# Kernel optimization log

Measured on AMD Instinct MI355X. Metric: run time of the kernel, lower is better.

The kernel has to match this reference:

```python
import jax, jax.numpy as jnp
import numpy as np
import math

D_MODEL = 2048
N_HEADS = 16
D_HEAD = D_MODEL // N_HEADS  # 128, also the RoPE dim
ROPE_BASE = 10000.0
B, T = 2, 2048


def _rope_cos_sin(seq_len, dim, dtype):
    inv_freq = 1.0 / (ROPE_BASE ** (jnp.arange(0, dim, 2, dtype=jnp.float32) / dim))
    t = jnp.arange(seq_len, dtype=jnp.float32)
    freqs = jnp.einsum('i,j->ij', t, inv_freq)          # [T, dim/2]
    emb = jnp.concatenate((freqs, freqs), axis=-1)       # [T, dim]  (half-concat layout, as in source)
    cos = jnp.cos(emb)[None, None, :, :].astype(dtype)   # [1,1,T,dim]
    sin = jnp.sin(emb)[None, None, :, :].astype(dtype)
    return cos, sin


def _apply_rot(x, cos, sin, dim):
    # interleaved pair rotation, faithful to the torch code
    x1 = x[..., 0:dim:2]
    x2 = x[..., 1:dim:2]
    x_rot = jnp.stack((-x2, x1), axis=-1).reshape(x.shape[:-1] + (dim,))
    return x[..., :dim] * cos + x_rot * sin


def setup_inputs() -> dict:
    key = jax.random.key(0)
    k1, k2, k3 = jax.random.split(key, 3)
    x = jax.random.normal(k1, (B, T, D_MODEL), dtype=jnp.float32)
    # causal additive mask, broadcastable to [B,H,T,T]
    neg = jnp.finfo(jnp.float32).min / 2
    causal = jnp.triu(jnp.full((T, T), neg, dtype=jnp.float32), k=1)
    mask = causal[None, None, :, :]
    Wqkv = jax.random.normal(k2, (D_MODEL, 3 * D_MODEL), dtype=jnp.float32) * (1.0 / math.sqrt(D_MODEL))
    bqkv = jnp.zeros((3 * D_MODEL,), dtype=jnp.float32)
    Wo = jax.random.normal(k3, (D_MODEL, D_MODEL), dtype=jnp.float32) * (1.0 / math.sqrt(D_MODEL))
    bo = jnp.zeros((D_MODEL,), dtype=jnp.float32)
    return {"x": x, "mask": mask, "Wqkv": Wqkv, "bqkv": bqkv, "Wo": Wo, "bo": bo}


def reference(x, mask, Wqkv, bqkv, Wo, bo):
    Bx, Tx, C = x.shape
    qkv = x @ Wqkv + bqkv                                     # [B,T,3C]
    qkv = qkv.reshape(Bx, Tx, 3, N_HEADS, D_HEAD)
    qkv = jnp.transpose(qkv, (2, 0, 3, 1, 4))                 # [3,B,H,T,dh]
    q, k, v = qkv[0], qkv[1], qkv[2]
    cos, sin = _rope_cos_sin(Tx, D_HEAD, x.dtype)
    q = _apply_rot(q, cos, sin, D_HEAD)
    k = _apply_rot(k, cos, sin, D_HEAD)
    att = jnp.einsum('bhqd,bhkd->bhqk', q, k) / math.sqrt(D_HEAD)
    att = att + mask
    att = jax.nn.softmax(att, axis=-1)
    y = jnp.einsum('bhqk,bhkd->bhqd', att, v)                 # [B,H,T,dh]
    y = jnp.transpose(y, (0, 2, 1, 3)).reshape(Bx, Tx, C)
    return y @ Wo + bo
```

## Files before the change

kernel.cpp:

```cpp
#include <hip/hip_runtime.h>
#include <stdint.h>

#define TDIM 2048
#define DMODEL 2048
#define NHEADS 16
#define DHEAD 128
#define NBATCH 2
#define NTOK (NBATCH * TDIM)
#define NQKV (3 * DMODEL)
#define BHTOT (NBATCH * NHEADS)

typedef unsigned short u16;
typedef __attribute__((ext_vector_type(8))) short bf16x8;
typedef __attribute__((ext_vector_type(4))) float f32x4;
typedef __attribute__((ext_vector_type(4))) int i32x4;

__device__ __forceinline__ u16 f2bf(float f) {
  union { float f; uint32_t u; } v; v.f = f;
  uint32_t u = v.u + 0x7fffu + ((v.u >> 16) & 1u);
  return (u16)(u >> 16);
}
__device__ __forceinline__ float bf2f(u16 h) {
  union { uint32_t u; float f; } v; v.u = ((uint32_t)h) << 16;
  return v.f;
}

#define GLOAD16(g, l)                                                        \
  __builtin_amdgcn_global_load_lds(                                          \
      (const __attribute__((address_space(1))) void*)(g),                    \
      (__attribute__((address_space(3))) void*)(l), 16, 0, 0)

__global__ void rope_table_kernel(float* __restrict__ ct, float* __restrict__ st) {
  int idx = blockIdx.x * 256 + threadIdx.x;
  int t = idx >> 6, m = idx & 63;
  float inv = expf(-(float)m * (9.210340371976184f / 64.0f));
  float ang = (float)t * inv;
  ct[idx] = cosf(ang);
  st[idx] = sinf(ang);
}

__global__ void convert_kernel(const float* __restrict__ in, u16* __restrict__ out) {
  int i = blockIdx.x * 256 + threadIdx.x;
  float4 v = ((const float4*)in)[i];
  ushort4 o;
  o.x = f2bf(v.x); o.y = f2bf(v.y); o.z = f2bf(v.z); o.w = f2bf(v.w);
  ((ushort4*)out)[i] = o;
}

__global__ __launch_bounds__(256) void transpose_convert_kernel(
    const float* __restrict__ in, u16* __restrict__ out, int K, int N) {
  __shared__ u16 tile[32][33];
  int n0 = blockIdx.x * 32, k0 = blockIdx.y * 32;
  int tx = threadIdx.x, ty = threadIdx.y;
  #pragma unroll
  for (int q = 0; q < 4; q++) {
    int k = ty + q * 8;
    tile[k][tx] = f2bf(in[(size_t)(k0 + k) * N + n0 + tx]);
  }
  __syncthreads();
  #pragma unroll
  for (int q = 0; q < 4; q++) {
    int n = ty + q * 8;
    out[(size_t)(n0 + n) * K + k0 + tx] = tile[tx][n];
  }
}

__global__ __launch_bounds__(256) void vtrans_kernel(
    const u16* __restrict__ Vtmp, u16* __restrict__ Vt) {
  __shared__ u16 tile[32][33];
  int bh = blockIdx.z;
  int t0 = blockIdx.x * 32, d0 = blockIdx.y * 32;
  int tx = threadIdx.x, ty = threadIdx.y;
  const u16* src = Vtmp + (size_t)bh * TDIM * DHEAD;
  u16* dst = Vt + (size_t)bh * DHEAD * TDIM;
  #pragma unroll
  for (int q = 0; q < 4; q++) {
    int t = ty + q * 8;
    tile[t][tx] = src[(size_t)(t0 + t) * DHEAD + d0 + tx];
  }
  __syncthreads();
  #pragma unroll
  for (int q = 0; q < 4; q++) {
    int d = ty + q * 8;
    dst[(size_t)(d0 + d) * TDIM + t0 + tx] = tile[tx][d];
  }
}

template <int MODE>
__global__ __launch_bounds__(512, 2) void gemm_bt_kernel(
    const u16* __restrict__ A, const u16* __restrict__ Bt,
    const float* __restrict__ bias,
    u16* __restrict__ q_out, u16* __restrict__ k_out, u16* __restrict__ v_out,
    float* __restrict__ f_out,
    const float* __restrict__ ct, const float* __restrict__ st, int K) {
  __shared__ __attribute__((aligned(128))) char lds[3][49152];
  const int tid = threadIdx.x;
  const int lane = tid & 63, w = tid >> 6;
  const int wr = w >> 2, wc = w & 3;
  const int g = lane >> 4, c = lane & 15;
  const int m0 = blockIdx.x * 128, n0 = blockIdx.y * 256;
  const size_t rowb = (size_t)K * 2;
  const int NKT = K >> 6;

  const char* sSrc[6]; int sDst[6];
  #pragma unroll
  for (int p = 0; p < 2; p++) {
    int o = p * 8192 + tid * 16;
    int row = o >> 7, j = (o >> 4) & 7;
    sSrc[p] = (const char*)A + (size_t)(m0 + row) * rowb + ((j ^ (row & 7)) << 4);
    sDst[p] = o;
  }
  #pragma unroll
  for (int p = 0; p < 4; p++) {
    int o = p * 8192 + tid * 16;
    int row = o >> 7, j = (o >> 4) & 7;
    sSrc[2 + p] = (const char*)Bt + (size_t)(n0 + row) * rowb + ((j ^ (row & 7)) << 4);
    sDst[2 + p] = 16384 + o;
  }

#define STAGE3(bufp, kt, base)                                               \
  {                                                                          \
    const size_t kb_ = (size_t)(kt) * 128;                                   \
    _Pragma("unroll") for (int p_ = 0; p_ < 3; p_++)                         \
        GLOAD16(sSrc[(base) + p_] + kb_, (bufp) + sDst[(base) + p_]);        \
  }

  int aRd[4][2], bRd[4][2];
  #pragma unroll
  for (int m = 0; m < 4; m++) {
    #pragma unroll
    for (int ks = 0; ks < 2; ks++) {
      int arow = wr * 64 + m * 16 + c;
      aRd[m][ks] = arow * 128 + (((ks * 4 + g) ^ (c & 7)) << 4);
      int brow = wc * 64 + m * 16 + c;
      bRd[m][ks] = 16384 + brow * 128 + (((ks * 4 + g) ^ (c & 7)) << 4);
    }
  }

  const f32x4 zero = {0.f, 0.f, 0.f, 0.f};
  f32x4 acc[4][4];
  #pragma unroll
  for (int m = 0; m < 4; m++)
    #pragma unroll
    for (int n = 0; n < 4; n++) acc[m][n] = zero;

  STAGE3(lds[0], 0, 0); STAGE3(lds[0], 0, 3);
  STAGE3(lds[1], 1, 0); STAGE3(lds[1], 1, 3);
  asm volatile("s_waitcnt vmcnt(6)" ::: "memory");
  __builtin_amdgcn_s_barrier();
  __builtin_amdgcn_sched_barrier(0);

  for (int kt = 0; kt < NKT; kt++) {
    char* bp = lds[kt % 3];
    char* sp = lds[(kt + 2) % 3];
    const bool do_stage = (kt + 2 < NKT);

    {
      bf16x8 afr[4], bfr[4];
      #pragma unroll
      for (int n = 0; n < 4; n++) bfr[n] = *(const bf16x8*)(bp + bRd[n][0]);
      #pragma unroll
      for (int m = 0; m < 4; m++) afr[m] = *(const bf16x8*)(bp + aRd[m][0]);
      if (do_stage) STAGE3(sp, kt + 2, 0);
      __builtin_amdgcn_s_barrier();
      asm volatile("s_waitcnt lgkmcnt(0)" ::: "memory");
      __builtin_amdgcn_sched_barrier(0);
      __builtin_amdgcn_s_setprio(1);
      #pragma unroll
      for (int m = 0; m < 4; m++)
        #pragma unroll
        for (int n = 0; n < 4; n++)
          acc[m][n] = __builtin_amdgcn_mfma_f32_16x16x32_bf16(
              afr[m], bfr[n], acc[m][n], 0, 0, 0);
      __builtin_amdgcn_s_setprio(0);
      __builtin_amdgcn_s_barrier();
      __builtin_amdgcn_sched_barrier(0);
    }

    {
      bf16x8 afr[4], bfr[4];
      #pragma unroll
      for (int n = 0; n < 4; n++) bfr[n] = *(const bf16x8*)(bp + bRd[n][1]);
      #pragma unroll
      for (int m = 0; m < 4; m++) afr[m] = *(const bf16x8*)(bp + aRd[m][1]);
      if (do_stage) STAGE3(sp, kt + 2, 3);
      if (do_stage) {
        asm volatile("s_waitcnt vmcnt(6)" ::: "memory");
      } else {
        asm volatile("s_waitcnt vmcnt(0)" ::: "memory");
      }
      __builtin_amdgcn_s_barrier();
      asm volatile("s_waitcnt lgkmcnt(0)" ::: "memory");
      __builtin_amdgcn_sched_barrier(0);
      __builtin_amdgcn_s_setprio(1);
      #pragma unroll
      for (int m = 0; m < 4; m++)
        #pragma unroll
        for (int n = 0; n < 4; n++)
          acc[m][n] = __builtin_amdgcn_mfma_f32_16x16x32_bf16(
              afr[m], bfr[n], acc[m][n], 0, 0, 0);
      __builtin_amdgcn_s_setprio(0);
      __builtin_amdgcn_s_barrier();
      __builtin_amdgcn_sched_barrier(0);
    }
  }
#undef STAGE3

  #pragma unroll
  for (int m = 0; m < 4; m++) {
    #pragma unroll
    for (int n = 0; n < 4; n++) {
      int gcol = n0 + wc * 64 + n * 16 + c;
      float bv = bias[gcol];
      float val[4];
      #pragma unroll
      for (int r = 0; r < 4; r++) val[r] = acc[m][n][r] + bv;
      if (MODE == 0) {
        int s = n0 >> 11;
        int rem = gcol & 2047;
        int h = rem >> 7, d = rem & 127;
        int b0 = (m0 + wr * 64 + m * 16) >> 11;
        size_t hb = (((size_t)(b0 * NHEADS + h)) * TDIM) * DHEAD + d;
        if (s == 2) {
          #pragma unroll
          for (int r = 0; r < 4; r++) {
            int t = (m0 + wr * 64 + m * 16 + g * 4 + r) & (TDIM - 1);
            v_out[hb + (size_t)t * DHEAD] = f2bf(val[r]);
          }
        } else {
          int mf = gcol & 63;
          float sgn = (c & 1) ? 1.0f : -1.0f;
          u16* dst = (s == 0) ? q_out : k_out;
          float qs = (s == 0) ? 0.08838834764831845f : 1.0f;
          #pragma unroll
          for (int r = 0; r < 4; r++) {
            float part = __shfl_xor(val[r], 1, 64);
            int t = (m0 + wr * 64 + m * 16 + g * 4 + r) & (TDIM - 1);
            float cs = ct[t * 64 + mf], sn = st[t * 64 + mf];
            float rot = (val[r] * cs + sgn * part * sn) * qs;
            dst[hb + (size_t)t * DHEAD] = f2bf(rot);
          }
        }
      } else {
        #pragma unroll
        for (int r = 0; r < 4; r++) {
          int grow = m0 + wr * 64 + m * 16 + g * 4 + r;
          f_out[(size_t)grow * DMODEL + gcol] = val[r];
        }
      }
    }
  }
}

__global__ __launch_bounds__(256) void attn_kernel(
    const u16* __restrict__ Q, const u16* __restrict__ K,
    const u16* __restrict__ Vt, u16* __restrict__ Yattn) {
  __shared__ u16 Ks[2][64 * 128];
  __shared__ u16 Vs[2][128 * 64];
  __shared__ u16 Ps[4][16 * 64];
  const int tid = threadIdx.x, lane = tid & 63, w = tid >> 6;
  const int g = lane >> 4, c = lane & 15;
  const int bh = blockIdx.y, b = bh >> 4, h = bh & 15;
  const u16* Qp = Q + (size_t)bh * TDIM * DHEAD;
  const u16* Kp = K + (size_t)bh * TDIM * DHEAD;
  const u16* Vp = Vt + (size_t)bh * DHEAD * TDIM;
  const f32x4 zero = {0.f, 0.f, 0.f, 0.f};

  for (int half = 0; half < 2; half++) {
    const int qt = half ? (31 - (int)blockIdx.x) : (int)blockIdx.x;
    const int qb = qt * 64 + w * 16;

    bf16x8 qf[4];
    #pragma unroll
    for (int kc = 0; kc < 4; kc++)
      qf[kc] = *(const bf16x8*)(Qp + (size_t)(qb + c) * DHEAD + kc * 32 + g * 8);

    f32x4 po[8];
    #pragma unroll
    for (int df = 0; df < 8; df++) po[df] = zero;
    float mrun[4], lrun[4];
    #pragma unroll
    for (int r = 0; r < 4; r++) { mrun[r] = -1e30f; lrun[r] = 0.f; }

    const int nt = qt + 1;

    {
      #pragma unroll
      for (int p = 0; p < 4; p++) {
        int off = p * 4096 + tid * 16;
        int kr = off >> 8, kc4 = (off & 255) >> 4;
        GLOAD16((const char*)Kp + (size_t)kr * 256 + ((kc4 ^ (kr & 7)) << 4),
                (char*)Ks[0] + off);
        int vr = off >> 7, vc4 = (off & 127) >> 4;
        GLOAD16((const char*)Vp + (size_t)vr * (TDIM * 2) + ((vc4 ^ (vr & 7)) << 4),
                (char*)Vs[0] + off);
      }
    }
    __syncthreads();

    int cur = 0;
    for (int t = 0; t < nt; t++) {
      if (t + 1 < nt) {
        int kv0n = (t + 1) * 64;
        char* KsN = (char*)Ks[cur ^ 1];
        char* VsN = (char*)Vs[cur ^ 1];
        #pragma unroll
        for (int p = 0; p < 4; p++) {
          int off = p * 4096 + tid * 16;
          int kr = off >> 8, kc4 = (off & 255) >> 4;
          GLOAD16((const char*)Kp + (size_t)(kv0n + kr) * 256 +
                      ((kc4 ^ (kr & 7)) << 4),
                  KsN + off);
          int vr = off >> 7, vc4 = (off & 127) >> 4;
          GLOAD16((const char*)Vp + (size_t)vr * (TDIM * 2) + (size_t)kv0n * 2 +
                      ((vc4 ^ (vr & 7)) << 4),
                  VsN + off);
        }
      }

      const u16* KsC = Ks[cur];
      const u16* VsC = Vs[cur];
      const int kv0 = t * 64;

      f32x4 sa[4];
      #pragma unroll
      for (int n = 0; n < 4; n++) sa[n] = zero;
      __builtin_amdgcn_s_setprio(1);
      #pragma unroll
      for (int n = 0; n < 4; n++) {
        int krow = n * 16 + c;
        #pragma unroll
        for (int kc = 0; kc < 4; kc++) {
          int kb = (kc * 32 + g * 8) * 2;
          bf16x8 kf = *(const bf16x8*)((const char*)KsC + krow * 256 +
                                       (kb ^ ((krow & 7) << 4)));
          sa[n] = __builtin_amdgcn_mfma_f32_16x16x32_bf16(qf[kc], kf, sa[n], 0, 0, 0);
        }
      }
      __builtin_amdgcn_s_setprio(0);

      if (kv0 + 63 > qb) {
        #pragma unroll
        for (int n = 0; n < 4; n++) {
          int col = kv0 + n * 16 + c;
          #pragma unroll
          for (int r = 0; r < 4; r++) {
            int qrow = qb + g * 4 + r;
            if (col > qrow) sa[n][r] = -1e30f;
          }
        }
      }

      float pvals[4][4];
      #pragma unroll
      for (int r = 0; r < 4; r++) {
        float vmax = fmaxf(fmaxf(sa[0][r], sa[1][r]), fmaxf(sa[2][r], sa[3][r]));
        #pragma unroll
        for (int d = 1; d < 16; d <<= 1) vmax = fmaxf(vmax, __shfl_xor(vmax, d, 64));
        float mnew = fmaxf(mrun[r], vmax);
        float scale = __expf(mrun[r] - mnew);
        float rs = 0.f;
        #pragma unroll
        for (int n = 0; n < 4; n++) {
          float p = __expf(sa[n][r] - mnew);
          pvals[r][n] = p;
          rs += p;
        }
        #pragma unroll
        for (int d = 1; d < 16; d <<= 1) rs += __shfl_xor(rs, d, 64);
        lrun[r] = lrun[r] * scale + rs;
        mrun[r] = mnew;
        #pragma unroll
        for (int df = 0; df < 8; df++) po[df][r] *= scale;
      }

      char* Pw = (char*)&Ps[w][0];
      #pragma unroll
      for (int r = 0; r < 4; r++) {
        int ri = g * 4 + r;
        #pragma unroll
        for (int n = 0; n < 4; n++) {
          int colb = (n * 16 + c) * 2;
          *(u16*)(Pw + ri * 128 + (colb ^ ((ri & 7) << 4))) = f2bf(pvals[r][n]);
        }
      }
      bf16x8 pa[2];
      #pragma unroll
      for (int kc2 = 0; kc2 < 2; kc2++) {
        int pb = (kc2 * 32 + g * 8) * 2;
        pa[kc2] = *(const bf16x8*)(Pw + c * 128 + (pb ^ ((c & 7) << 4)));
      }
      __builtin_amdgcn_s_setprio(1);
      #pragma unroll
      for (int df = 0; df < 8; df++) {
        #pragma unroll
        for (int kc2 = 0; kc2 < 2; kc2++) {
          int vrow = df * 16 + c;
          int vb = (kc2 * 32 + g * 8) * 2;
          bf16x8 vf = *(const bf16x8*)((const char*)VsC + vrow * 128 +
                                       (vb ^ ((vrow & 7) << 4)));
          po[df] = __builtin_amdgcn_mfma_f32_16x16x32_bf16(pa[kc2], vf, po[df], 0, 0, 0);
        }
      }
      __builtin_amdgcn_s_setprio(0);

      __syncthreads();
      cur ^= 1;
    }

    float inv[4];
    #pragma unroll
    for (int r = 0; r < 4; r++) inv[r] = 1.0f / lrun[r];
    #pragma unroll
    for (int df = 0; df < 8; df++) {
      #pragma unroll
      for (int r = 0; r < 4; r++) {
        int trow = qb + g * 4 + r;
        int col = h * DHEAD + df * 16 + c;
        Yattn[((size_t)b * TDIM + trow) * DMODEL + col] = f2bf(po[df][r] * inv[r]);
      }
    }
  }
}

extern "C" void kernel_launch(void* const* d_in, const int* in_sizes, int n_in,
                              void* d_out, int out_size, void* d_ws, size_t ws_size,
                              hipStream_t stream) {
  const float* x    = (const float*)d_in[0];
  const float* Wqkv = (const float*)d_in[2];
  const float* bqkv = (const float*)d_in[3];
  const float* Wo   = (const float*)d_in[4];
  const float* bo   = (const float*)d_in[5];
  float* out = (float*)d_out;

  char* ws = (char*)d_ws;
  size_t o = 0;
  u16* xb    = (u16*)(ws + o); o += (size_t)NTOK * DMODEL * 2;
  u16* Wqkvt = (u16*)(ws + o); o += (size_t)NQKV * DMODEL * 2;
  u16* Wot   = (u16*)(ws + o); o += (size_t)DMODEL * DMODEL * 2;
  u16* Qb    = (u16*)(ws + o); o += (size_t)BHTOT * TDIM * DHEAD * 2;
  u16* Kb    = (u16*)(ws + o); o += (size_t)BHTOT * TDIM * DHEAD * 2;
  u16* Vtmp  = (u16*)(ws + o); o += (size_t)BHTOT * TDIM * DHEAD * 2;
  float* ct  = (float*)(ws + o); o += (size_t)TDIM * 64 * 4;
  float* st  = (float*)(ws + o); o += (size_t)TDIM * 64 * 4;
  u16* Vt    = xb;
  u16* Yattn = Vtmp;

  dim3 tb32x8(32, 8);

  rope_table_kernel<<<(TDIM * 64) / 256, 256, 0, stream>>>(ct, st);
  convert_kernel<<<(NTOK * DMODEL / 4) / 256, 256, 0, stream>>>(x, xb);
  transpose_convert_kernel<<<dim3(NQKV / 32, DMODEL / 32), tb32x8, 0, stream>>>(
      Wqkv, Wqkvt, DMODEL, NQKV);
  transpose_convert_kernel<<<dim3(DMODEL / 32, DMODEL / 32), tb32x8, 0, stream>>>(
      Wo, Wot, DMODEL, DMODEL);

  gemm_bt_kernel<0><<<dim3(NTOK / 128, NQKV / 256), 512, 0, stream>>>(
      xb, Wqkvt, bqkv, Qb, Kb, Vtmp, nullptr, ct, st, DMODEL);

  vtrans_kernel<<<dim3(TDIM / 32, DHEAD / 32, BHTOT), tb32x8, 0, stream>>>(Vtmp, Vt);

  attn_kernel<<<dim3(16, BHTOT), 256, 0, stream>>>(Qb, Kb, Vt, Yattn);

  gemm_bt_kernel<1><<<dim3(NTOK / 128, DMODEL / 256), 512, 0, stream>>>(
      Yattn, Wot, bo, nullptr, nullptr, nullptr, out, nullptr, nullptr, DMODEL);
}
```

Before: 294.7 us.

## Enlarge GEMM tile to 256x256 with double-buffered quadrant-interleaved pipeline

The bf16 GEMM block tile grows from 128x256 to 256x256, so each warp computes a 128x64 output (8x4 MFMA fragments) instead of 64x64. The three-buffer LDS ring is replaced by two 64KB buffers, and each k-tile is split into four MFMA quadrant phases with the next tile's half-loads interleaved between them. This raises arithmetic intensity and reduces global/LDS traffic per FLOP. In exchange it doubles the accumulator registers, uses 128KB of LDS, and halves the grid size (QKV 384 blocks, out-proj 128), which can hurt occupancy and wave balance on 256 CUs.

```diff
diff --git a/kernel.cpp b/kernel.cpp
--- a/kernel.cpp
+++ b/kernel.cpp
@@ -93,124 +93,163 @@
     u16* __restrict__ q_out, u16* __restrict__ k_out, u16* __restrict__ v_out,
     float* __restrict__ f_out,
     const float* __restrict__ ct, const float* __restrict__ st, int K) {
-  __shared__ __attribute__((aligned(128))) char lds[3][49152];
+  __shared__ __attribute__((aligned(128))) char lds[2][65536];
   const int tid = threadIdx.x;
   const int lane = tid & 63, w = tid >> 6;
   const int wr = w >> 2, wc = w & 3;
   const int g = lane >> 4, c = lane & 15;
-  const int m0 = blockIdx.x * 128, n0 = blockIdx.y * 256;
+  const int m0 = blockIdx.x * 256, n0 = blockIdx.y * 256;
   const size_t rowb = (size_t)K * 2;
   const int NKT = K >> 6;
-
-  const char* sSrc[6]; int sDst[6];
+  const size_t R64 = (size_t)64 * rowb;
+
+  const int srow = tid >> 3, sj = tid & 7;
+  const char* aP = (const char*)A + (size_t)(m0 + srow) * rowb +
+                   ((sj ^ (srow & 7)) << 4);
+  const char* bP = (const char*)Bt + (size_t)(n0 + srow) * rowb +
+                   ((sj ^ (srow & 7)) << 4);
+
+#define STAGE_H(tb, basePtr, rowoff, destoff, ktgt)                          \
+  {                                                                          \
+    const char* s_ = (basePtr) + (size_t)(rowoff) * rowb +                   \
+                     (size_t)(ktgt) * 128;                                   \
+    GLOAD16(s_, lds[tb] + (destoff) + (tid << 4));                           \
+    GLOAD16(s_ + R64, lds[tb] + (destoff) + 8192 + (tid << 4));              \
+  }
+
+  const int xk0 = (g ^ (c & 7)) << 4;
+  const int xk1 = ((g + 4) ^ (c & 7)) << 4;
+  const int aBase = wr * 16384 + c * 128;
+  const int bBase = 32768 + (wc >> 1) * 16384 + ((wc & 1) * 64 + c) * 128;
+
+  const f32x4 zero = {0.f, 0.f, 0.f, 0.f};
+  f32x4 acc[8][4];
   #pragma unroll
-  for (int p = 0; p < 2; p++) {
-    int o = p * 8192 + tid * 16;
-    int row = o >> 7, j = (o >> 4) & 7;
-    sSrc[p] = (const char*)A + (size_t)(m0 + row) * rowb + ((j ^ (row & 7)) << 4);
-    sDst[p] = o;
-  }
-  #pragma unroll
-  for (int p = 0; p < 4; p++) {
-    int o = p * 8192 + tid * 16;
-    int row = o >> 7, j = (o >> 4) & 7;
-    sSrc[2 + p] = (const char*)Bt + (size_t)(n0 + row) * rowb + ((j ^ (row & 7)) << 4);
-    sDst[2 + p] = 16384 + o;
-  }
-
-#define STAGE3(bufp, kt, base)                                               \
-  {                                                                          \
-    const size_t kb_ = (size_t)(kt) * 128;                                   \
-    _Pragma("unroll") for (int p_ = 0; p_ < 3; p_++)                         \
-        GLOAD16(sSrc[(base) + p_] + kb_, (bufp) + sDst[(base) + p_]);        \
-  }
-
-  int aRd[4][2], bRd[4][2];
-  #pragma unroll
-  for (int m = 0; m < 4; m++) {
-    #pragma unroll
-    for (int ks = 0; ks < 2; ks++) {
-      int arow = wr * 64 + m * 16 + c;
-      aRd[m][ks] = arow * 128 + (((ks * 4 + g) ^ (c & 7)) << 4);
-      int brow = wc * 64 + m * 16 + c;
-      bRd[m][ks] = 16384 + brow * 128 + (((ks * 4 + g) ^ (c & 7)) << 4);
-    }
-  }
-
-  const f32x4 zero = {0.f, 0.f, 0.f, 0.f};
-  f32x4 acc[4][4];
-  #pragma unroll
-  for (int m = 0; m < 4; m++)
+  for (int m = 0; m < 8; m++)
     #pragma unroll
     for (int n = 0; n < 4; n++) acc[m][n] = zero;
 
-  STAGE3(lds[0], 0, 0); STAGE3(lds[0], 0, 3);
-  STAGE3(lds[1], 1, 0); STAGE3(lds[1], 1, 3);
-  asm volatile("s_waitcnt vmcnt(6)" ::: "memory");
+  STAGE_H(0, aP, 0, 0, 0);
+  STAGE_H(0, aP, 128, 16384, 0);
+  STAGE_H(0, bP, 0, 32768, 0);
+  STAGE_H(0, bP, 128, 49152, 0);
+  if (NKT > 1) {
+    STAGE_H(1, aP, 0, 0, 1);
+    STAGE_H(1, aP, 128, 16384, 1);
+    asm volatile("s_waitcnt vmcnt(4)" ::: "memory");
+  } else {
+    asm volatile("s_waitcnt vmcnt(0)" ::: "memory");
+  }
   __builtin_amdgcn_s_barrier();
   __builtin_amdgcn_sched_barrier(0);
 
   for (int kt = 0; kt < NKT; kt++) {
-    char* bp = lds[kt % 3];
-    char* sp = lds[(kt + 2) % 3];
-    const bool do_stage = (kt + 2 < NKT);
-
-    {
-      bf16x8 afr[4], bfr[4];
-      #pragma unroll
-      for (int n = 0; n < 4; n++) bfr[n] = *(const bf16x8*)(bp + bRd[n][0]);
-      #pragma unroll
-      for (int m = 0; m < 4; m++) afr[m] = *(const bf16x8*)(bp + aRd[m][0]);
-      if (do_stage) STAGE3(sp, kt + 2, 0);
-      __builtin_amdgcn_s_barrier();
-      asm volatile("s_waitcnt lgkmcnt(0)" ::: "memory");
-      __builtin_amdgcn_sched_barrier(0);
-      __builtin_amdgcn_s_setprio(1);
+    const char* bp = (const char*)lds[kt & 1];
+    const int nb = (kt + 1) & 1;
+    bf16x8 aLo[4][2], aHi[4][2], bLo[2][2], bHi[2][2];
+
+    #pragma unroll
+    for (int m = 0; m < 4; m++) {
+      aLo[m][0] = *(const bf16x8*)(bp + aBase + m * 2048 + xk0);
+      aLo[m][1] = *(const bf16x8*)(bp + aBase + m * 2048 + xk1);
+    }
+    #pragma unroll
+    for (int n = 0; n < 2; n++) {
+      bLo[n][0] = *(const bf16x8*)(bp + bBase + n * 2048 + xk0);
+      bLo[n][1] = *(const bf16x8*)(bp + bBase + n * 2048 + xk1);
+    }
+    if (kt + 1 < NKT) STAGE_H(nb, bP, 0, 32768, kt + 1);
+    __builtin_amdgcn_s_barrier();
+    asm volatile("s_waitcnt lgkmcnt(0)" ::: "memory");
+    __builtin_amdgcn_sched_barrier(0);
+    __builtin_amdgcn_s_setprio(1);
+    #pragma unroll
+    for (int ks = 0; ks < 2; ks++)
       #pragma unroll
       for (int m = 0; m < 4; m++)
         #pragma unroll
-        for (int n = 0; n < 4; n++)
+        for (int n = 0; n < 2; n++)
           acc[m][n] = __builtin_amdgcn_mfma_f32_16x16x32_bf16(
-              afr[m], bfr[n], acc[m][n], 0, 0, 0);
-      __builtin_amdgcn_s_setprio(0);
-      __builtin_amdgcn_s_barrier();
-      __builtin_amdgcn_sched_barrier(0);
-    }
-
-    {
-      bf16x8 afr[4], bfr[4];
-      #pragma unroll
-      for (int n = 0; n < 4; n++) bfr[n] = *(const bf16x8*)(bp + bRd[n][1]);
-      #pragma unroll
-      for (int m = 0; m < 4; m++) afr[m] = *(const bf16x8*)(bp + aRd[m][1]);
-      if (do_stage) STAGE3(sp, kt + 2, 3);
-      if (do_stage) {
-        asm volatile("s_waitcnt vmcnt(6)" ::: "memory");
+              aLo[m][ks], bLo[n][ks], acc[m][n], 0, 0, 0);
+    __builtin_amdgcn_s_setprio(0);
+    __builtin_amdgcn_s_barrier();
+    __builtin_amdgcn_sched_barrier(0);
+
+    #pragma unroll
+    for (int m = 0; m < 4; m++) {
+      aHi[m][0] = *(const bf16x8*)(bp + aBase + (m + 4) * 2048 + xk0);
+      aHi[m][1] = *(const bf16x8*)(bp + aBase + (m + 4) * 2048 + xk1);
+    }
+    if (kt + 1 < NKT) STAGE_H(nb, bP, 128, 49152, kt + 1);
+    __builtin_amdgcn_s_barrier();
+    asm volatile("s_waitcnt lgkmcnt(0)" ::: "memory");
+    __builtin_amdgcn_sched_barrier(0);
+    __builtin_amdgcn_s_setprio(1);
+    #pragma unroll
+    for (int ks = 0; ks < 2; ks++)
+      #pragma unroll
+      for (int m = 0; m < 4; m++)
+        #pragma unroll
+        for (int n = 0; n < 2; n++)
+          acc[m + 4][n] = __builtin_amdgcn_mfma_f32_16x16x32_bf16(
+              aHi[m][ks], bLo[n][ks], acc[m + 4][n], 0, 0, 0);
+    __builtin_amdgcn_s_setprio(0);
+    __builtin_amdgcn_s_barrier();
+    __builtin_amdgcn_sched_barrier(0);
+
+    #pragma unroll
+    for (int n = 0; n < 2; n++) {
+      bHi[n][0] = *(const bf16x8*)(bp + bBase + (n + 2) * 2048 + xk0);
+      bHi[n][1] = *(const bf16x8*)(bp + bBase + (n + 2) * 2048 + xk1);
+    }
+    if (kt + 2 < NKT) STAGE_H(kt & 1, aP, 0, 0, kt + 2);
+    __builtin_amdgcn_s_barrier();
+    asm volatile("s_waitcnt lgkmcnt(0)" ::: "memory");
+    __builtin_amdgcn_sched_barrier(0);
+    __builtin_amdgcn_s_setprio(1);
+    #pragma unroll
+    for (int ks = 0; ks < 2; ks++)
+      #pragma unroll
+      for (int m = 0; m < 4; m++)
+        #pragma unroll
+        for (int n = 0; n < 2; n++)
+          acc[m + 4][n + 2] = __builtin_amdgcn_mfma_f32_16x16x32_bf16(
+              aHi[m][ks], bHi[n][ks], acc[m + 4][n + 2], 0, 0, 0);
+    __builtin_amdgcn_s_setprio(0);
+    __builtin_amdgcn_s_barrier();
+    __builtin_amdgcn_sched_barrier(0);
+
+    if (kt + 2 < NKT) STAGE_H(kt & 1, aP, 128, 16384, kt + 2);
+    if (kt + 1 < NKT) {
+      if (kt + 2 < NKT) {
+        asm volatile("s_waitcnt vmcnt(4)" ::: "memory");
       } else {
         asm volatile("s_waitcnt vmcnt(0)" ::: "memory");
       }
-      __builtin_amdgcn_s_barrier();
-      asm volatile("s_waitcnt lgkmcnt(0)" ::: "memory");
-      __builtin_amdgcn_sched_barrier(0);
-      __builtin_amdgcn_s_setprio(1);
+    }
+    __builtin_amdgcn_s_barrier();
+    __builtin_amdgcn_sched_barrier(0);
+    __builtin_amdgcn_s_setprio(1);
+    #pragma unroll
+    for (int ks = 0; ks < 2; ks++)
       #pragma unroll
       for (int m = 0; m < 4; m++)
         #pragma unroll
-        for (int n = 0; n < 4; n++)
-          acc[m][n] = __builtin_amdgcn_mfma_f32_16x16x32_bf16(
-              afr[m], bfr[n], acc[m][n], 0, 0, 0);
-      __builtin_amdgcn_s_setprio(0);
-      __builtin_amdgcn_s_barrier();
-      __builtin_amdgcn_sched_barrier(0);
-    }
-  }
-#undef STAGE3
+        for (int n = 0; n < 2; n++)
+          acc[m][n + 2] = __builtin_amdgcn_mfma_f32_16x16x32_bf16(
+              aLo[m][ks], bHi[n][ks], acc[m][n + 2], 0, 0, 0);
+    __builtin_amdgcn_s_setprio(0);
+    __builtin_amdgcn_s_barrier();
+    __builtin_amdgcn_sched_barrier(0);
+  }
+#undef STAGE_H
 
   #pragma unroll
-  for (int m = 0; m < 4; m++) {
+  for (int m = 0; m < 8; m++) {
     #pragma unroll
     for (int n = 0; n < 4; n++) {
       int gcol = n0 + wc * 64 + n * 16 + c;
+      int growb = m0 + wr * 128 + m * 16;
       float bv = bias[gcol];
       float val[4];
       #pragma unroll
@@ -219,12 +258,12 @@
         int s = n0 >> 11;
         int rem = gcol & 2047;
         int h = rem >> 7, d = rem & 127;
-        int b0 = (m0 + wr * 64 + m * 16) >> 11;
+        int b0 = growb >> 11;
         size_t hb = (((size_t)(b0 * NHEADS + h)) * TDIM) * DHEAD + d;
         if (s == 2) {
           #pragma unroll
           for (int r = 0; r < 4; r++) {
-            int t = (m0 + wr * 64 + m * 16 + g * 4 + r) & (TDIM - 1);
+            int t = (growb + g * 4 + r) & (TDIM - 1);
             v_out[hb + (size_t)t * DHEAD] = f2bf(val[r]);
           }
         } else {
@@ -235,7 +274,7 @@
           #pragma unroll
           for (int r = 0; r < 4; r++) {
             float part = __shfl_xor(val[r], 1, 64);
-            int t = (m0 + wr * 64 + m * 16 + g * 4 + r) & (TDIM - 1);
+            int t = (growb + g * 4 + r) & (TDIM - 1);
             float cs = ct[t * 64 + mf], sn = st[t * 64 + mf];
             float rot = (val[r] * cs + sgn * part * sn) * qs;
             dst[hb + (size_t)t * DHEAD] = f2bf(rot);
@@ -244,7 +283,7 @@
       } else {
         #pragma unroll
         for (int r = 0; r < 4; r++) {
-          int grow = m0 + wr * 64 + m * 16 + g * 4 + r;
+          int grow = growb + g * 4 + r;
           f_out[(size_t)grow * DMODEL + gcol] = val[r];
         }
       }
@@ -455,13 +494,13 @@
   transpose_convert_kernel<<<dim3(DMODEL / 32, DMODEL / 32), tb32x8, 0, stream>>>(
       Wo, Wot, DMODEL, DMODEL);
 
-  gemm_bt_kernel<0><<<dim3(NTOK / 128, NQKV / 256), 512, 0, stream>>>(
+  gemm_bt_kernel<0><<<dim3(NTOK / 256, NQKV / 256), 512, 0, stream>>>(
       xb, Wqkvt, bqkv, Qb, Kb, Vtmp, nullptr, ct, st, DMODEL);
 
   vtrans_kernel<<<dim3(TDIM / 32, DHEAD / 32, BHTOT), tb32x8, 0, stream>>>(Vtmp, Vt);
 
   attn_kernel<<<dim3(16, BHTOT), 256, 0, stream>>>(Qb, Kb, Vt, Yattn);
 
-  gemm_bt_kernel<1><<<dim3(NTOK / 128, DMODEL / 256), 512, 0, stream>>>(
+  gemm_bt_kernel<1><<<dim3(NTOK / 256, DMODEL / 256), 512, 0, stream>>>(
       Yattn, Wot, bo, nullptr, nullptr, nullptr, out, nullptr, nullptr, DMODEL);
 }
```

New measurement: 318.8 us. +8.2%, slower.
